# Performance work log

Measured on AMD Instinct MI355X. Metric: run time of the kernel, lower is better.

The kernel has to match this reference:

```python
import jax, jax.numpy as jnp
import numpy as np

EMBED_DIM = 1024
NUM_HEADS = 16
HEAD_DIM = EMBED_DIM // NUM_HEADS
B, N = 4, 2048


def setup_inputs() -> dict:
    key = jax.random.key(0)
    k = jax.random.split(key, 5)
    s = 1.0 / np.sqrt(EMBED_DIM)
    return {
        "x": jax.random.normal(k[0], (B, N, EMBED_DIM), dtype=jnp.float32),
        "W_qkv": jax.random.uniform(k[1], (EMBED_DIM, 3 * EMBED_DIM), jnp.float32, -s, s),
        "b_qkv": jax.random.uniform(k[2], (3 * EMBED_DIM,), jnp.float32, -s, s),
        "W_proj": jax.random.uniform(k[3], (EMBED_DIM, EMBED_DIM), jnp.float32, -s, s),
        "b_proj": jax.random.uniform(k[4], (EMBED_DIM,), jnp.float32, -s, s),
    }


def reference(x, W_qkv, b_qkv, W_proj, b_proj):
    b, n, c = x.shape
    qkv = x @ W_qkv + b_qkv                       # [B,N,3C]
    qkv = qkv.reshape(b, n, 3, NUM_HEADS, HEAD_DIM)
    q = qkv[:, :, 0].transpose(0, 2, 1, 3)        # [B,H,N,D]
    k = qkv[:, :, 1].transpose(0, 2, 1, 3)
    v = qkv[:, :, 2].transpose(0, 2, 1, 3)
    scale = 1.0 / np.sqrt(HEAD_DIM).astype(np.float32)
    scores = jnp.einsum("bhqd,bhkd->bhqk", q, k) * scale
    attn = jax.nn.softmax(scores, axis=-1)
    out = jnp.einsum("bhqk,bhkd->bhqd", attn, v)  # [B,H,N,D]
    out = out.transpose(0, 2, 1, 3).reshape(b, n, c)
    return out @ W_proj + b_proj
```

## Files before the change

kernel.cpp:

```cpp
#include <hip/hip_runtime.h>
#include <math.h>


typedef __bf16 bf16x8 __attribute__((ext_vector_type(8)));
typedef float f32x4 __attribute__((ext_vector_type(4)));

#define EMBED 1024
#define NHEAD 16
#define BATCH 4
#define SEQ 2048
#define M_TOT 8192
#define QKV_N 3072
#define QSCALE 0.18033688011112042f

__device__ __forceinline__ ushort f2bf(float f) {
  union { float f; unsigned u; } x; x.f = f;
  unsigned r = x.u + 0x7FFFu + ((x.u >> 16) & 1u);
  return (ushort)(r >> 16);
}

__device__ __forceinline__ uint cvt2bf(float a, float b) {
#if __has_builtin(__builtin_amdgcn_cvt_pk_bf16_f32)
  typedef __bf16 bf16x2 __attribute__((ext_vector_type(2)));
  union { bf16x2 v; uint u; } c;
  c.v = __builtin_amdgcn_cvt_pk_bf16_f32(a, b);
  return c.u;
#else
  return (uint)f2bf(a) | ((uint)f2bf(b) << 16);
#endif
}

__device__ __forceinline__ float fexp2(float x) {
#if __has_builtin(__builtin_amdgcn_exp2f)
  return __builtin_amdgcn_exp2f(x);
#else
  return exp2f(x);
#endif
}

__device__ __forceinline__ f32x4 mfma16(bf16x8 a, bf16x8 b, f32x4 c) {
  return __builtin_amdgcn_mfma_f32_16x16x32_bf16(a, b, c, 0, 0, 0);
}

__device__ __forceinline__ void gl2lds16(const void* g, void* l) {
  __builtin_amdgcn_global_load_lds(
      (const __attribute__((address_space(1))) unsigned int*)g,
      (__attribute__((address_space(3))) unsigned int*)l, 16, 0, 0);
}

__global__ __launch_bounds__(256) void prep_kernel(
    const float* __restrict__ x, ushort* __restrict__ xb,
    const float* __restrict__ Wqkv, ushort* __restrict__ Wqkv_t,
    const float* __restrict__ Wproj, ushort* __restrict__ Wproj_t) {
  __shared__ float tile[64][65];
  const int bid = blockIdx.x;
  const int t = threadIdx.x;
  if (bid < 8192) {
    int i = (bid * 256 + t) * 4;
    float4 v = *reinterpret_cast<const float4*>(&x[i]);
    uint2 w = {cvt2bf(v.x, v.y), cvt2bf(v.z, v.w)};
    *reinterpret_cast<uint2*>(&xb[i]) = w;
    return;
  }
  const float* in;
  ushort* out;
  int Kd = 1024, Nd, n0, k0;
  if (bid < 8960) {
    int b2 = bid - 8192;
    in = Wqkv; out = Wqkv_t; Nd = 3072;
    n0 = (b2 % 48) * 64; k0 = (b2 / 48) * 64;
  } else {
    int b2 = bid - 8960;
    in = Wproj; out = Wproj_t; Nd = 1024;
    n0 = (b2 % 16) * 64; k0 = (b2 / 16) * 64;
  }
#pragma unroll
  for (int i = 0; i < 16; ++i) {
    int e = t + 256 * i;
    int kr = e >> 6, nc = e & 63;
    tile[kr][nc] = in[(size_t)(k0 + kr) * Nd + n0 + nc];
  }
  __syncthreads();
#pragma unroll
  for (int i = 0; i < 16; ++i) {
    int e = t + 256 * i;
    int nr = e >> 6, kc = e & 63;
    out[(size_t)(n0 + nr) * Kd + k0 + kc] = f2bf(tile[kc][nr]);
  }
}

__global__ __launch_bounds__(256) void gemm_bf16(
    const ushort* __restrict__ A, const ushort* __restrict__ Bt,
    const float* __restrict__ bias, void* __restrict__ Cout,
    ushort* __restrict__ vtgout, int M, int N, int K, int mode) {
  __shared__ ushort As[128 * 64];
  __shared__ ushort Bs[128 * 64];
  const int t = threadIdx.x;
  const int wave = t >> 6, lane = t & 63;
  const int lane15 = lane & 15, quad = lane >> 4;
  const int m0 = blockIdx.y * 128, n0 = blockIdx.x * 128;
  const int wm = (wave >> 1) * 64, wn = (wave & 1) * 64;

  int srow[4], scol[4], sdst[4];
#pragma unroll
  for (int j = 0; j < 4; ++j) {
    int c = (j * 4 + wave) * 64 + lane;
    int row = c >> 3;
    scol[j] = ((c & 7) ^ (row & 7)) * 8;
    srow[j] = row;
    sdst[j] = (j * 4 + wave) * 512;
  }
  const int sw = lane15 & 7;

  f32x4 acc[4][4] = {};

  for (int k0 = 0; k0 < K; k0 += 64) {
#pragma unroll
    for (int j = 0; j < 4; ++j) {
      gl2lds16(&A[(size_t)(m0 + srow[j]) * K + k0 + scol[j]], &As[sdst[j]]);
      gl2lds16(&Bt[(size_t)(n0 + srow[j]) * K + k0 + scol[j]], &Bs[sdst[j]]);
    }
    __syncthreads();

#pragma unroll
    for (int kk = 0; kk < 2; ++kk) {
      bf16x8 af[4], bfr[4];
#pragma unroll
      for (int ms = 0; ms < 4; ++ms)
        af[ms] = *reinterpret_cast<const bf16x8*>(
            &As[(wm + ms * 16 + lane15) * 64 + (((kk * 4 + quad) ^ sw) * 8)]);
#pragma unroll
      for (int ns = 0; ns < 4; ++ns)
        bfr[ns] = *reinterpret_cast<const bf16x8*>(
            &Bs[(wn + ns * 16 + lane15) * 64 + (((kk * 4 + quad) ^ sw) * 8)]);
#pragma unroll
      for (int ms = 0; ms < 4; ++ms)
#pragma unroll
        for (int ns = 0; ns < 4; ++ns)
          acc[ms][ns] = mfma16(af[ms], bfr[ns], acc[ms][ns]);
    }
    __syncthreads();
  }

  if (mode == 0) {
    float* out = (float*)Cout;
#pragma unroll
    for (int ns = 0; ns < 4; ++ns) {
      int col = n0 + wn + ns * 16 + lane15;
      float bv = bias[col];
#pragma unroll
      for (int ms = 0; ms < 4; ++ms)
#pragma unroll
        for (int r = 0; r < 4; ++r) {
          int row = m0 + wm + ms * 16 + quad * 4 + r;
          out[(size_t)row * N + col] = acc[ms][ns][r] + bv;
        }
    }
  } else {
    ushort* qk = (ushort*)Cout;
#pragma unroll
    for (int ns = 0; ns < 4; ++ns) {
      int col = n0 + wn + ns * 16 + lane15;
      float bv = bias[col];
      if (col < 2048) {
        float sc = (col < 1024) ? QSCALE : 1.0f;
#pragma unroll
        for (int ms = 0; ms < 4; ++ms) {
          int row = m0 + wm + ms * 16 + quad * 4;
          uint u01 = cvt2bf((acc[ms][ns][0] + bv) * sc, (acc[ms][ns][1] + bv) * sc);
          uint u23 = cvt2bf((acc[ms][ns][2] + bv) * sc, (acc[ms][ns][3] + bv) * sc);
          qk[(size_t)(row + 0) * 2048 + col] = (ushort)u01;
          qk[(size_t)(row + 1) * 2048 + col] = (ushort)(u01 >> 16);
          qk[(size_t)(row + 2) * 2048 + col] = (ushort)u23;
          qk[(size_t)(row + 3) * 2048 + col] = (ushort)(u23 >> 16);
        }
      } else {
        int dp = col - 2048;
#pragma unroll
        for (int ms = 0; ms < 4; ++ms) {
          int row = m0 + wm + ms * 16 + quad * 4;
          int b = row >> 11, seq = row & 2047;
          uint2 w = {cvt2bf(acc[ms][ns][0] + bv, acc[ms][ns][1] + bv),
                     cvt2bf(acc[ms][ns][2] + bv, acc[ms][ns][3] + bv)};
          *reinterpret_cast<uint2*>(
              &vtgout[((size_t)(b * 1024 + dp) << 11) + seq]) = w;
        }
      }
    }
  }
}

#define QG 2

__global__ __launch_bounds__(256, 4) void attn_kernel(
    const ushort* __restrict__ qk, const ushort* __restrict__ vtg,
    ushort* __restrict__ out) {
  __shared__ ushort Ks[2][4096];
  __shared__ ushort Vt[2][4096];
  __shared__ ushort Ps[4][16 * 64];

  const int t = threadIdx.x;
  const int wave = t >> 6, lane = t & 63;
  const int lane15 = lane & 15, quad = lane >> 4;
  const int bh = blockIdx.x, qg = blockIdx.y;
  const int b = bh >> 4, h = bh & 15;
  const size_t boff = (size_t)b * SEQ * 2048;

  int sdst[2];
  const ushort* kptr[2];
  const ushort* vptr[2];
#pragma unroll
  for (int j = 0; j < 2; ++j) {
    int lg = (j * 4 + wave) * 64 + lane;
    int row = lg >> 3;
    int col = ((lg & 7) ^ (row & 7)) * 8;
    sdst[j] = (j * 4 + wave) * 512;
    kptr[j] = qk + boff + (size_t)row * 2048 + 1024 + h * 64 + col;
    vptr[j] = vtg + ((size_t)(b * 1024 + h * 64 + row) << 11) + col;
  }

  bf16x8 qf[QG][2];
#pragma unroll
  for (int g = 0; g < QG; ++g) {
    size_t qoff = boff +
        (size_t)(qg * (QG * 64) + g * 64 + wave * 16 + lane15) * 2048 + h * 64;
    qf[g][0] = *reinterpret_cast<const bf16x8*>(&qk[qoff + quad * 8]);
    qf[g][1] = *reinterpret_cast<const bf16x8*>(&qk[qoff + 32 + quad * 8]);
  }

  bf16x8 ones;
#pragma unroll
  for (int j = 0; j < 8; ++j) ones[j] = (__bf16)1.0f;

  f32x4 O[QG][4] = {};
  f32x4 lacc[QG] = {};
  const int sw = lane15 & 7;
  ushort* ps = Ps[wave];

#pragma unroll
  for (int j = 0; j < 2; ++j) {
    gl2lds16(kptr[j], &Ks[0][sdst[j]]);
    gl2lds16(vptr[j], &Vt[0][sdst[j]]);
  }
  __syncthreads();

  for (int kt = 0; kt < SEQ / 64; ++kt) {
    const int cur = kt & 1, nxt = cur ^ 1;
    if (kt < SEQ / 64 - 1) {
#pragma unroll
      for (int j = 0; j < 2; ++j) {
        gl2lds16(kptr[j] + (size_t)(kt + 1) * 64 * 2048, &Ks[nxt][sdst[j]]);
        gl2lds16(vptr[j] + (kt + 1) * 64, &Vt[nxt][sdst[j]]);
      }
    }

    bf16x8 kf[4][2], vf[2][4];
#pragma unroll
    for (int nsub = 0; nsub < 4; ++nsub) {
      const int kr = (nsub * 16 + lane15) * 64;
      kf[nsub][0] = *reinterpret_cast<const bf16x8*>(
          &Ks[cur][kr + ((quad ^ sw) * 8)]);
      kf[nsub][1] = *reinterpret_cast<const bf16x8*>(
          &Ks[cur][kr + (((quad + 4) ^ sw) * 8)]);
    }
#pragma unroll
    for (int kk = 0; kk < 2; ++kk)
#pragma unroll
      for (int dsub = 0; dsub < 4; ++dsub) {
        int d = dsub * 16 + lane15;
        vf[kk][dsub] = *reinterpret_cast<const bf16x8*>(
            &Vt[cur][d * 64 + (((kk * 4 + quad) ^ sw) * 8)]);
      }

#pragma unroll
    for (int g = 0; g < QG; ++g) {
      f32x4 st[4];
#pragma unroll
      for (int nsub = 0; nsub < 4; ++nsub) {
        f32x4 a = {-32.0f, -32.0f, -32.0f, -32.0f};
        a = mfma16(kf[nsub][0], qf[g][0], a);
        a = mfma16(kf[nsub][1], qf[g][1], a);
        st[nsub] = a;
      }
#pragma unroll
      for (int nsub = 0; nsub < 4; ++nsub) {
        uint2 w = {cvt2bf(fexp2(st[nsub][0]), fexp2(st[nsub][1])),
                   cvt2bf(fexp2(st[nsub][2]), fexp2(st[nsub][3]))};
        *reinterpret_cast<uint2*>(
            &ps[lane15 * 64 + (((2 * nsub + (quad >> 1)) ^ sw) << 3) +
                ((quad & 1) << 2)]) = w;
      }
#pragma unroll
      for (int kk = 0; kk < 2; ++kk) {
        bf16x8 pf = *reinterpret_cast<const bf16x8*>(
            &ps[lane15 * 64 + (((kk * 4 + quad) ^ sw) << 3)]);
#pragma unroll
        for (int dsub = 0; dsub < 4; ++dsub)
          O[g][dsub] = mfma16(pf, vf[kk][dsub], O[g][dsub]);
        lacc[g] = mfma16(pf, ones, lacc[g]);
      }
    }
    __syncthreads();
  }

#pragma unroll
  for (int g = 0; g < QG; ++g)
#pragma unroll
    for (int r = 0; r < 4; ++r) {
      float linv = __builtin_amdgcn_rcpf(lacc[g][r]);
      size_t rowoff =
          (size_t)(b * SEQ + qg * (QG * 64) + g * 64 + wave * 16 + quad * 4 +
                   r) * EMBED + h * 64;
      uint u01 = cvt2bf(O[g][0][r] * linv, O[g][1][r] * linv);
      uint u23 = cvt2bf(O[g][2][r] * linv, O[g][3][r] * linv);
      out[rowoff + 0 * 16 + lane15] = (ushort)u01;
      out[rowoff + 1 * 16 + lane15] = (ushort)(u01 >> 16);
      out[rowoff + 2 * 16 + lane15] = (ushort)u23;
      out[rowoff + 3 * 16 + lane15] = (ushort)(u23 >> 16);
    }
}

extern "C" void kernel_launch(void* const* d_in, const int* in_sizes, int n_in,
                              void* d_out, int out_size, void* d_ws,
                              size_t ws_size, hipStream_t stream) {
  const float* x = (const float*)d_in[0];
  const float* Wqkv = (const float*)d_in[1];
  const float* bqkv = (const float*)d_in[2];
  const float* Wproj = (const float*)d_in[3];
  const float* bproj = (const float*)d_in[4];
  float* out = (float*)d_out;

  char* ws = (char*)d_ws;
  ushort* Wqkv_t = (ushort*)ws;
  ushort* Wproj_t = (ushort*)(ws + 6291456);
  ushort* qk = (ushort*)(ws + 8388608);
  ushort* vtg = (ushort*)(ws + 41943040);
  ushort* xb = (ushort*)(ws + 58720256);
  ushort* attnout = (ushort*)(ws + 58720256);

  prep_kernel<<<8192 + 768 + 256, 256, 0, stream>>>(
      x, xb, Wqkv, Wqkv_t, Wproj, Wproj_t);
  gemm_bf16<<<dim3(QKV_N / 128, M_TOT / 128), 256, 0, stream>>>(
      xb, Wqkv_t, bqkv, qk, vtg, M_TOT, QKV_N, EMBED, 1);
  attn_kernel<<<dim3(NHEAD * BATCH, SEQ / (QG * 64)), 256, 0, stream>>>(
      qk, vtg, attnout);
  gemm_bf16<<<dim3(EMBED / 128, M_TOT / 128), 256, 0, stream>>>(
      attnout, Wproj_t, bproj, out, nullptr, M_TOT, EMBED, EMBED, 0);
}
```

Before: 292.5 us.

## Halve attention key tile to 32 and raise occupancy with MFMA priority hints

Shrinks the attention kernel's per-iteration key/value tile from 64 to 32 keys, which halves the LDS buffers for K, V^T and P. Launch bounds rise from 4 to 5 blocks per CU, and the V and P swizzles are redone for the narrower rows. s_setprio is placed around the MFMA sections so waves doing matrix work get scheduling priority. The trade-off is twice as many loop iterations and barriers, and fewer MFMAs per sync, in exchange for more resident waves to hide latency.

New measurement: 440.9 us. 50.8% more time.

```diff
diff --git a/kernel.cpp b/kernel.cpp
--- a/kernel.cpp
+++ b/kernel.cpp
@@ -192,12 +192,12 @@
 
 #define QG 2
 
-__global__ __launch_bounds__(256, 4) void attn_kernel(
+__global__ __launch_bounds__(256, 5) void attn_kernel(
     const ushort* __restrict__ qk, const ushort* __restrict__ vtg,
     ushort* __restrict__ out) {
-  __shared__ ushort Ks[2][4096];
-  __shared__ ushort Vt[2][4096];
-  __shared__ ushort Ps[4][16 * 64];
+  __shared__ ushort Ks[2][2048];
+  __shared__ ushort Vt[2][2048];
+  __shared__ ushort Ps[4][512];
 
   const int t = threadIdx.x;
   const int wave = t >> 6, lane = t & 63;
@@ -206,18 +206,12 @@
   const int b = bh >> 4, h = bh & 15;
   const size_t boff = (size_t)b * SEQ * 2048;
 
-  int sdst[2];
-  const ushort* kptr[2];
-  const ushort* vptr[2];
-#pragma unroll
-  for (int j = 0; j < 2; ++j) {
-    int lg = (j * 4 + wave) * 64 + lane;
-    int row = lg >> 3;
-    int col = ((lg & 7) ^ (row & 7)) * 8;
-    sdst[j] = (j * 4 + wave) * 512;
-    kptr[j] = qk + boff + (size_t)row * 2048 + 1024 + h * 64 + col;
-    vptr[j] = vtg + ((size_t)(b * 1024 + h * 64 + row) << 11) + col;
-  }
+  const int lg = wave * 64 + lane;
+  const int krow = lg >> 3, kc = ((lg & 7) ^ (krow & 7)) * 8;
+  const int vrow = lg >> 2, vc = ((lg & 3) ^ ((vrow >> 1) & 3)) * 8;
+  const ushort* kp = qk + boff + (size_t)krow * 2048 + 1024 + h * 64 + kc;
+  const ushort* vp = vtg + ((size_t)(b * 1024 + h * 64 + vrow) << 11) + vc;
+  const int sdst = wave * 512;
 
   bf16x8 qf[QG][2];
 #pragma unroll
@@ -235,28 +229,23 @@
   f32x4 O[QG][4] = {};
   f32x4 lacc[QG] = {};
   const int sw = lane15 & 7;
+  const int psw = (lane15 >> 1) & 3;
   ushort* ps = Ps[wave];
 
-#pragma unroll
-  for (int j = 0; j < 2; ++j) {
-    gl2lds16(kptr[j], &Ks[0][sdst[j]]);
-    gl2lds16(vptr[j], &Vt[0][sdst[j]]);
-  }
+  gl2lds16(kp, &Ks[0][sdst]);
+  gl2lds16(vp, &Vt[0][sdst]);
   __syncthreads();
 
-  for (int kt = 0; kt < SEQ / 64; ++kt) {
+  for (int kt = 0; kt < SEQ / 32; ++kt) {
     const int cur = kt & 1, nxt = cur ^ 1;
-    if (kt < SEQ / 64 - 1) {
-#pragma unroll
-      for (int j = 0; j < 2; ++j) {
-        gl2lds16(kptr[j] + (size_t)(kt + 1) * 64 * 2048, &Ks[nxt][sdst[j]]);
-        gl2lds16(vptr[j] + (kt + 1) * 64, &Vt[nxt][sdst[j]]);
-      }
-    }
-
-    bf16x8 kf[4][2], vf[2][4];
-#pragma unroll
-    for (int nsub = 0; nsub < 4; ++nsub) {
+    if (kt < SEQ / 32 - 1) {
+      gl2lds16(kp + (size_t)(kt + 1) * 32 * 2048, &Ks[nxt][sdst]);
+      gl2lds16(vp + (kt + 1) * 32, &Vt[nxt][sdst]);
+    }
+
+    bf16x8 kf[2][2], vf[4];
+#pragma unroll
+    for (int nsub = 0; nsub < 2; ++nsub) {
       const int kr = (nsub * 16 + lane15) * 64;
       kf[nsub][0] = *reinterpret_cast<const bf16x8*>(
           &Ks[cur][kr + ((quad ^ sw) * 8)]);
@@ -264,41 +253,40 @@
           &Ks[cur][kr + (((quad + 4) ^ sw) * 8)]);
     }
 #pragma unroll
-    for (int kk = 0; kk < 2; ++kk)
-#pragma unroll
-      for (int dsub = 0; dsub < 4; ++dsub) {
-        int d = dsub * 16 + lane15;
-        vf[kk][dsub] = *reinterpret_cast<const bf16x8*>(
-            &Vt[cur][d * 64 + (((kk * 4 + quad) ^ sw) * 8)]);
-      }
+    for (int dsub = 0; dsub < 4; ++dsub) {
+      int d = dsub * 16 + lane15;
+      vf[dsub] = *reinterpret_cast<const bf16x8*>(
+          &Vt[cur][d * 32 + ((quad ^ psw) * 8)]);
+    }
 
 #pragma unroll
     for (int g = 0; g < QG; ++g) {
-      f32x4 st[4];
-#pragma unroll
-      for (int nsub = 0; nsub < 4; ++nsub) {
+      f32x4 st[2];
+      __builtin_amdgcn_s_setprio(1);
+#pragma unroll
+      for (int nsub = 0; nsub < 2; ++nsub) {
         f32x4 a = {-32.0f, -32.0f, -32.0f, -32.0f};
         a = mfma16(kf[nsub][0], qf[g][0], a);
         a = mfma16(kf[nsub][1], qf[g][1], a);
         st[nsub] = a;
       }
-#pragma unroll
-      for (int nsub = 0; nsub < 4; ++nsub) {
+      __builtin_amdgcn_s_setprio(0);
+#pragma unroll
+      for (int nsub = 0; nsub < 2; ++nsub) {
         uint2 w = {cvt2bf(fexp2(st[nsub][0]), fexp2(st[nsub][1])),
                    cvt2bf(fexp2(st[nsub][2]), fexp2(st[nsub][3]))};
         *reinterpret_cast<uint2*>(
-            &ps[lane15 * 64 + (((2 * nsub + (quad >> 1)) ^ sw) << 3) +
+            &ps[lane15 * 32 + (((2 * nsub + (quad >> 1)) ^ psw) << 3) +
                 ((quad & 1) << 2)]) = w;
       }
-#pragma unroll
-      for (int kk = 0; kk < 2; ++kk) {
-        bf16x8 pf = *reinterpret_cast<const bf16x8*>(
-            &ps[lane15 * 64 + (((kk * 4 + quad) ^ sw) << 3)]);
-#pragma unroll
-        for (int dsub = 0; dsub < 4; ++dsub)
-          O[g][dsub] = mfma16(pf, vf[kk][dsub], O[g][dsub]);
-        lacc[g] = mfma16(pf, ones, lacc[g]);
-      }
+      bf16x8 pf = *reinterpret_cast<const bf16x8*>(
+          &ps[lane15 * 32 + ((quad ^ psw) << 3)]);
+      __builtin_amdgcn_s_setprio(1);
+#pragma unroll
+      for (int dsub = 0; dsub < 4; ++dsub)
+        O[g][dsub] = mfma16(pf, vf[dsub], O[g][dsub]);
+      lacc[g] = mfma16(pf, ones, lacc[g]);
+      __builtin_amdgcn_s_setprio(0);
     }
     __syncthreads();
   }
```
